# Kernel optimization log

Measured on AMD Instinct MI355X. Metric: run time of the kernel, lower is better.

Reference implementation:

```python
import jax, jax.numpy as jnp
import numpy as np

B, S, D, H, FFN = 2, 2048, 1024, 8, 4096
DK = D // H            # head key/query dim = 128
VD = 2 * D             # double_v_dim -> v_dim = 2048
DV = VD // H           # per-head value dim = 256
SCALE_BASE = 512.0
EPS = 1e-5


def _dup_interleave(m):
    # (S, d/2) -> (S, d), each column repeated twice adjacently
    return jnp.repeat(m, 2, axis=-1)


def _rotate_every_two(x):
    x1 = x[..., 0::2]
    x2 = x[..., 1::2]
    return jnp.stack((-x2, x1), axis=-1).reshape(x.shape)


def _xpos(x, downscale):
    # x: (B,H,S,d) -- XPOS rotary with length-dependent scale
    d = x.shape[-1]
    pos = jnp.arange(x.shape[-2], dtype=jnp.float32)
    sv = (jnp.arange(0, d, 2, dtype=jnp.float32) + 0.4 * d) / (1.4 * d)  # (d/2,)
    scale = sv[None, :] ** (pos / SCALE_BASE)[:, None]                    # (S, d/2)
    half = d // 2
    inv_freq = 1.0 / (10000.0 ** (jnp.arange(half, dtype=jnp.float32) / half))
    sinusoid = pos[:, None] * inv_freq[None, :]                           # (S, d/2)
    if downscale:
        scale = 1.0 / scale
    sin = _dup_interleave(jnp.sin(sinusoid) * scale)                      # (S, d)
    cos = _dup_interleave(jnp.cos(sinusoid) * scale)
    return x * cos + _rotate_every_two(x) * sin


def _gammas(heads):
    return 1.0 - jnp.exp(jnp.linspace(np.log(1 / 32), np.log(1 / 512), heads)).astype(jnp.float32)


def _layernorm(x, w, b):
    mu = jnp.mean(x, axis=-1, keepdims=True)
    var = jnp.var(x, axis=-1, keepdims=True)
    return (x - mu) * jax.lax.rsqrt(var + EPS) * w + b


def setup_inputs() -> dict:
    key = jax.random.key(0)
    ks = jax.random.split(key, 16)
    sD = 1.0 / np.sqrt(D)
    sF = 1.0 / np.sqrt(FFN)
    return {
        "X": jax.random.normal(ks[0], (B, S, D), jnp.float32),
        "Wq": jax.random.normal(ks[1], (H, D, DK), jnp.float32) * sD,
        "Wk": jax.random.normal(ks[2], (H, D, DK), jnp.float32) * sD,
        "Wv": jax.random.normal(ks[3], (H, D, DV), jnp.float32) * sD,
        "W_G": jax.random.normal(ks[4], (D, VD), jnp.float32) * sD,
        "W_O": jax.random.normal(ks[5], (VD, D), jnp.float32) / np.sqrt(VD),
        "gn_w": jnp.ones((VD,), jnp.float32),
        "gn_b": jnp.zeros((VD,), jnp.float32),
        "ln1_w": jnp.ones((D,), jnp.float32),
        "ln1_b": jnp.zeros((D,), jnp.float32),
        "ln2_w": jnp.ones((D,), jnp.float32),
        "ln2_b": jnp.zeros((D,), jnp.float32),
        "ffn_w1": jax.random.normal(ks[6], (D, FFN), jnp.float32) * sD,
        "ffn_b1": jnp.zeros((FFN,), jnp.float32),
        "ffn_w2": jax.random.normal(ks[7], (FFN, D), jnp.float32) * sF,
        "ffn_b2": jnp.zeros((D,), jnp.float32),
    }


def _retention(Xn, Wq, Wk, Wv, W_G, W_O, gn_w, gn_b):
    # Xn: (B,S,D) pre-normalized input
    Q = jnp.einsum("bsd,hdk->bhsk", Xn, Wq)
    K = jnp.einsum("bsd,hdk->bhsk", Xn, Wk)
    V = jnp.einsum("bsd,hdv->bhsv", Xn, Wv)
    Q = _xpos(Q, downscale=False)
    K = _xpos(K, downscale=True)
    # decay matrix D[h,n,m] = gamma_h^(n-m) for n>=m else 0
    n = jnp.arange(S)[:, None]
    m = jnp.arange(S)[None, :]
    mask = (n >= m)
    exponent = jnp.where(mask, (n - m).astype(jnp.float32), 0.0)
    g = _gammas(H)
    Dmat = jnp.where(mask[None], g[:, None, None] ** exponent[None], 0.0)  # (H,S,S)
    ret = jnp.einsum("bhsk,bhtk->bhst", Q, K) * Dmat[None]
    Y = jnp.einsum("bhst,bhtv->bhsv", ret, V)                              # (B,H,S,DV)
    Y = jnp.transpose(Y, (0, 2, 1, 3))                                     # (B,S,H,DV)
    # GroupNorm(heads, v_dim) applied per token: normalize within each head chunk
    mu = jnp.mean(Y, axis=-1, keepdims=True)
    var = jnp.var(Y, axis=-1, keepdims=True)
    Y = (Y - mu) * jax.lax.rsqrt(var + EPS)
    Y = Y.reshape(B, S, VD) * gn_w + gn_b
    G = Xn @ W_G
    gated = (G * jax.nn.sigmoid(G)) * Y                                     # swish gate
    return gated @ W_O


def reference(X, Wq, Wk, Wv, W_G, W_O, gn_w, gn_b, ln1_w, ln1_b, ln2_w, ln2_b,
              ffn_w1, ffn_b1, ffn_w2, ffn_b2):
    X = _retention(_layernorm(X, ln1_w, ln1_b), Wq, Wk, Wv, W_G, W_O, gn_w, gn_b) + X
    h = _layernorm(X, ln2_w, ln2_b)
    h = jax.nn.gelu(h @ ffn_w1 + ffn_b1, approximate=False) @ ffn_w2 + ffn_b2
    return h + X
```

## Files before the change

kernel.cpp:

```cpp
#include <hip/hip_runtime.h>
#include <hip/hip_bf16.h>

typedef unsigned short u16;
typedef unsigned int   u32;
typedef short short8 __attribute__((ext_vector_type(8)));
typedef float f32x4  __attribute__((ext_vector_type(4)));

__device__ __forceinline__ float b2f(u16 u) { return __uint_as_float(((u32)u) << 16); }
__device__ __forceinline__ u16 f2b(float f) {
    u32 u = __float_as_uint(f);
    u += 0x7FFF + ((u >> 16) & 1);
    return (u16)(u >> 16);
}

typedef const unsigned int __attribute__((address_space(1)))* gas1;
typedef unsigned int __attribute__((address_space(3)))* las3;
__device__ __forceinline__ void async_ld16(const void* g, const void* l) {
    __builtin_amdgcn_global_load_lds((gas1)(unsigned long long)g,
                                     (las3)(unsigned int)(unsigned long long)l,
                                     16, 0, 0);
}

__device__ __forceinline__ void wtrans_body(const float* __restrict__ W, u16* __restrict__ Wt,
                                            int K, int N, int bx, int by, int bz) {
    __shared__ u16 tile[32][36];
    const int k0 = bx * 32, n0 = by * 32;
    const float* Wz = W + (long)bz * K * N;
    u16* Wtz = Wt + (long)bz * K * N;
    const int t = threadIdx.x;
    const int r = t >> 3, c = (t & 7) * 4;
    float4 v = *(const float4*)(Wz + (long)(k0 + r) * N + n0 + c);
    tile[r][c+0] = f2b(v.x); tile[r][c+1] = f2b(v.y);
    tile[r][c+2] = f2b(v.z); tile[r][c+3] = f2b(v.w);
    __syncthreads();
    uint2 pk;
    pk.x = (u32)tile[c+0][r] | ((u32)tile[c+1][r] << 16);
    pk.y = (u32)tile[c+2][r] | ((u32)tile[c+3][r] << 16);
    *(uint2*)(Wtz + (long)(n0 + r) * K + k0 + c) = pk;
}

__device__ __forceinline__ void xtab_body(float4* __restrict__ tab, int blk) {
    int idx = blk * 256 + threadIdx.x;
    int j = idx & 63, s = idx >> 6;
    float sv = (2.f * j + 51.2f) / 179.2f;
    float scale = exp2f(log2f(sv) * ((float)s * (1.f / 512.f)));
    float inv_freq = exp2f((float)j * (-13.287712379549449f / 64.f));
    float ang = (float)s * inv_freq;
    float sn = sinf(ang), cs = cosf(ang);
    tab[idx] = make_float4(cs * scale, sn * scale, cs / scale, sn / scale);
}

__device__ __forceinline__ void ln_body(const float* __restrict__ X,
                                        const float* __restrict__ w,
                                        const float* __restrict__ bb,
                                        u16* __restrict__ out, long row) {
    const int t = threadIdx.x;
    float4 p = ((const float4*)(X + row * 1024))[t];
    float x[4] = { p.x, p.y, p.z, p.w };
    float s = x[0]+x[1]+x[2]+x[3];
    float q = x[0]*x[0]+x[1]*x[1]+x[2]*x[2]+x[3]*x[3];
#pragma unroll
    for (int o = 32; o > 0; o >>= 1) { s += __shfl_down(s, o, 64); q += __shfl_down(q, o, 64); }
    __shared__ float aS[4], aQ[4];
    if ((t & 63) == 0) { aS[t >> 6] = s; aQ[t >> 6] = q; }
    __syncthreads();
    s = aS[0]+aS[1]+aS[2]+aS[3];
    q = aQ[0]+aQ[1]+aQ[2]+aQ[3];
    float mean = s * (1.f/1024.f);
    float var  = q * (1.f/1024.f) - mean*mean;
    float rstd = rsqrtf(var + 1e-5f);
    float4 wv = ((const float4*)w)[t];
    float4 bv = ((const float4*)bb)[t];
    uint2 r;
    r.x = (u32)f2b((x[0]-mean)*rstd*wv.x + bv.x) | ((u32)f2b((x[1]-mean)*rstd*wv.y + bv.y) << 16);
    r.y = (u32)f2b((x[2]-mean)*rstd*wv.z + bv.z) | ((u32)f2b((x[3]-mean)*rstd*wv.w + bv.w) << 16);
    ((uint2*)(out + row * 1024))[t] = r;
}

__global__ __launch_bounds__(256) void prep_k(
    const float* __restrict__ Wq, const float* __restrict__ Wk,
    const float* __restrict__ Wv, const float* __restrict__ WG,
    const float* __restrict__ WO, const float* __restrict__ fw1,
    const float* __restrict__ fw2, const float* __restrict__ X,
    const float* __restrict__ ln1w, const float* __restrict__ ln1b,
    u16* __restrict__ WT, u16* __restrict__ WOT,
    u16* __restrict__ fw1T, u16* __restrict__ fw2T,
    float4* __restrict__ xtab, u16* __restrict__ Xn) {
    const int id = blockIdx.x;
    if (id < 16384) {
        const float* W; u16* Wt; int K, N, bx, by, bz = 0;
        if (id < 1024)       { W=Wq;  Wt=WT;           K=1024; N=128;  int l=id;       bx=l&31;  by=(l>>5)&3; bz=l>>7; }
        else if (id < 2048)  { W=Wk;  Wt=WT+1048576;   K=1024; N=128;  int l=id-1024;  bx=l&31;  by=(l>>5)&3; bz=l>>7; }
        else if (id < 4096)  { W=Wv;  Wt=WT+2097152;   K=1024; N=256;  int l=id-2048;  bx=l&31;  by=(l>>5)&7; bz=l>>8; }
        else if (id < 6144)  { W=WG;  Wt=WT+4194304;   K=1024; N=2048; int l=id-4096;  bx=l&31;  by=l>>5; }
        else if (id < 8192)  { W=WO;  Wt=WOT;          K=2048; N=1024; int l=id-6144;  bx=l&63;  by=l>>6; }
        else if (id < 12288) { W=fw1; Wt=fw1T;         K=1024; N=4096; int l=id-8192;  bx=l&31;  by=l>>5; }
        else                 { W=fw2; Wt=fw2T;         K=4096; N=1024; int l=id-12288; bx=l&127; by=l>>7; }
        wtrans_body(W, Wt, K, N, bx, by, bz);
    } else if (id < 16896) {
        xtab_body(xtab, id - 16384);
    } else {
        ln_body(X, ln1w, ln1b, Xn, id - 16896);
    }
}

__global__ __launch_bounds__(256) void ln2_combine(const float* __restrict__ P,
                                                   const float* __restrict__ X,
                                                   const float* __restrict__ w,
                                                   const float* __restrict__ bb,
                                                   float* __restrict__ X2,
                                                   u16* __restrict__ hb) {
    const long row = blockIdx.x;
    const int t = threadIdx.x;
    const float* p = P + row * 3072;
    float4 a = ((const float4*)p)[t];
    float4 c = ((const float4*)(p + 1024))[t];
    float4 xr = ((const float4*)(X + row * 1024))[t];
    float x[4] = { a.x+c.x+xr.x, a.y+c.y+xr.y, a.z+c.z+xr.z, a.w+c.w+xr.w };
    ((float4*)(X2 + row * 1024))[t] = make_float4(x[0], x[1], x[2], x[3]);
    float s = x[0]+x[1]+x[2]+x[3];
    float q = x[0]*x[0]+x[1]*x[1]+x[2]*x[2]+x[3]*x[3];
#pragma unroll
    for (int o = 32; o > 0; o >>= 1) { s += __shfl_down(s, o, 64); q += __shfl_down(q, o, 64); }
    __shared__ float aS[4], aQ[4];
    if ((t & 63) == 0) { aS[t >> 6] = s; aQ[t >> 6] = q; }
    __syncthreads();
    s = aS[0]+aS[1]+aS[2]+aS[3];
    q = aQ[0]+aQ[1]+aQ[2]+aQ[3];
    float mean = s * (1.f/1024.f);
    float var  = q * (1.f/1024.f) - mean*mean;
    float rstd = rsqrtf(var + 1e-5f);
    float4 wv = ((const float4*)w)[t];
    float4 bv = ((const float4*)bb)[t];
    uint2 r;
    r.x = (u32)f2b((x[0]-mean)*rstd*wv.x + bv.x) | ((u32)f2b((x[1]-mean)*rstd*wv.y + bv.y) << 16);
    r.y = (u32)f2b((x[2]-mean)*rstd*wv.z + bv.z) | ((u32)f2b((x[3]-mean)*rstd*wv.w + bv.w) << 16);
    ((uint2*)(hb + row * 1024))[t] = r;
}

__global__ __launch_bounds__(256) void ffn2_combine(const float* __restrict__ P,
                                                    const float* __restrict__ b2,
                                                    const float* __restrict__ X2,
                                                    float* __restrict__ out) {
    const long row = blockIdx.x;
    const int t = threadIdx.x;
    float4 p0 = ((const float4*)(P + row * 1024))[t];
    float4 p1 = ((const float4*)(P + 16777216 + row * 1024))[t];
    float4 x2 = ((const float4*)(X2 + row * 1024))[t];
    float4 bv = ((const float4*)b2)[t];
    ((float4*)(out + row * 1024))[t] = make_float4(
        p0.x + p1.x + x2.x + bv.x, p0.y + p1.y + x2.y + bv.y,
        p0.z + p1.z + x2.z + bv.z, p0.w + p1.w + x2.w + bv.w);
}

__global__ __launch_bounds__(256) void vtrans(const u16* __restrict__ Vseg, u16* __restrict__ Vt) {
    __shared__ u16 tile[32][36];
    const int s0 = blockIdx.x * 32, v0 = blockIdx.y * 32, z = blockIdx.z;
    const int b = z >> 3, h = z & 7;
    const u16* Vz = Vseg + (long)b * 2048 * 6144 + h * 256;
    u16* Vtz = Vt + (long)z * 256 * 2048;
    const int t = threadIdx.x;
    const int r = t >> 3, c = (t & 7) * 4;
    uint2 ld = *(const uint2*)(Vz + (long)(s0 + r) * 6144 + v0 + c);
    tile[r][c+0] = (u16)(ld.x & 0xFFFF); tile[r][c+1] = (u16)(ld.x >> 16);
    tile[r][c+2] = (u16)(ld.y & 0xFFFF); tile[r][c+3] = (u16)(ld.y >> 16);
    __syncthreads();
    uint2 pk;
    pk.x = (u32)tile[c+0][r] | ((u32)tile[c+1][r] << 16);
    pk.y = (u32)tile[c+2][r] | ((u32)tile[c+3][r] << 16);
    *(uint2*)(Vtz + (long)(v0 + r) * 2048 + s0 + c) = pk;
}

enum { EPI_GELU_BIAS = 2, EPI_QKVG = 4 };

template<int EPI>
__global__ __launch_bounds__(256) void mgemm(
    const u16* __restrict__ A, const u16* __restrict__ Bt, u16* __restrict__ Cv,
    int K, int aStride, long cStride,
    const float* __restrict__ bias) {
    __shared__ __align__(16) u16 As[2 * 128 * 32];
    __shared__ __align__(16) u16 Bs[2 * 128 * 32];
    const int pid = blockIdx.x;
    const int mb = pid & 31;
    const int nb = pid >> 5;
    const int t = threadIdx.x;
    const int row0 = mb * 128, col0 = nb * 128;
    const int wave = t >> 6, lane = t & 63;
    const int wm = wave >> 1, wn = wave & 1;
    const int quad = lane >> 4, l16 = lane & 15;
    const u16* Ag = A + (long)(row0 + (t >> 2)) * aStride + ((t & 3) * 8);
    const u16* Bg = Bt + (long)(col0 + (t >> 2)) * K + ((t & 3) * 8);
    const long aj = (long)64 * aStride;
    const long bj = (long)64 * K;
    const u32 lo = __builtin_amdgcn_readfirstlane((u32)(wave * 1024));

    f32x4 acc[4][4];
#pragma unroll
    for (int i = 0; i < 4; i++)
#pragma unroll
        for (int j = 0; j < 4; j++) acc[i][j] = (f32x4){0.f, 0.f, 0.f, 0.f};

    for (int k0 = 0; k0 < K; k0 += 64) {
#pragma unroll
        for (int h = 0; h < 2; h++) {
            const u16* Agh = Ag + k0 + h * 32;
            const u16* Bgh = Bg + k0 + h * 32;
            async_ld16(Agh,      (const char*)As + h*8192 + lo);
            async_ld16(Agh + aj, (const char*)As + h*8192 + 4096 + lo);
            async_ld16(Bgh,      (const char*)Bs + h*8192 + lo);
            async_ld16(Bgh + bj, (const char*)Bs + h*8192 + 4096 + lo);
        }
        __syncthreads();
#pragma unroll
        for (int h = 0; h < 2; h++) {
            short8 af[4], bf[4];
#pragma unroll
            for (int mt = 0; mt < 4; mt++)
                af[mt] = *(const short8*)(As + h*4096 + (wm*64 + mt*16 + l16) * 32 + quad*8);
#pragma unroll
            for (int nt = 0; nt < 4; nt++)
                bf[nt] = *(const short8*)(Bs + h*4096 + (wn*64 + nt*16 + l16) * 32 + quad*8);
#pragma unroll
            for (int mt = 0; mt < 4; mt++)
#pragma unroll
                for (int nt = 0; nt < 4; nt++)
                    acc[mt][nt] = __builtin_amdgcn_mfma_f32_16x16x32_bf16(af[mt], bf[nt], acc[mt][nt], 0, 0, 0);
        }
        __syncthreads();
    }

#pragma unroll
    for (int mt = 0; mt < 4; mt++) {
#pragma unroll
        for (int reg = 0; reg < 4; reg++) {
            int r = row0 + wm*64 + mt*16 + quad*4 + reg;
#pragma unroll
            for (int nt = 0; nt < 4; nt++) {
                int c = col0 + wn*64 + nt*16 + l16;
                float v = acc[mt][nt][reg];
                if constexpr (EPI == EPI_GELU_BIAS) {
                    v += bias[c];
                    v = 0.5f * v * (1.f + erff(v * 0.70710678118654752f));
                }
                float pv = __shfl_xor(v, 1, 64);
                float w0 = v, w1 = pv;
                if constexpr (EPI == EPI_QKVG) {
                    if (c < 2048) {
                        int j = (c & 127) >> 1;
                        float4 tb = ((const float4*)bias)[((r & 2047) << 6) + j];
                        float cs = (c < 1024) ? tb.x : tb.z;
                        float sn = (c < 1024) ? tb.y : tb.w;
                        w0 = v * cs - pv * sn;
                        w1 = pv * cs + v * sn;
                    }
                }
                if (!(lane & 1)) {
                    u32 pk = (u32)f2b(w0) | ((u32)f2b(w1) << 16);
                    *(u32*)(Cv + (long)r * cStride + c) = pk;
                }
            }
        }
    }
}

__global__ __launch_bounds__(256) void mgemm_sk(
    const u16* __restrict__ A, const u16* __restrict__ Bt, float* __restrict__ P,
    int K, int kHalf, int aStride, long pRowStride, long sliceOff) {
    __shared__ __align__(16) u16 As[2 * 128 * 32];
    __shared__ __align__(16) u16 Bs[2 * 128 * 32];
    const int pid = blockIdx.x;
    const int mb = pid & 31;
    const int nb = (pid & 255) >> 5;
    const int slice = pid >> 8;
    const int t = threadIdx.x;
    const int row0 = mb * 128, col0 = nb * 128;
    const int wave = t >> 6, lane = t & 63;
    const int wm = wave >> 1, wn = wave & 1;
    const int quad = lane >> 4, l16 = lane & 15;
    const u16* Ag = A + (long)(row0 + (t >> 2)) * aStride + ((t & 3) * 8);
    const u16* Bg = Bt + (long)(col0 + (t >> 2)) * K + ((t & 3) * 8);
    const long aj = (long)64 * aStride;
    const long bj = (long)64 * K;
    const u32 lo = __builtin_amdgcn_readfirstlane((u32)(wave * 1024));

    f32x4 acc[4][4];
#pragma unroll
    for (int i = 0; i < 4; i++)
#pragma unroll
        for (int j = 0; j < 4; j++) acc[i][j] = (f32x4){0.f, 0.f, 0.f, 0.f};

    const int kBeg = slice * kHalf, kEnd = kBeg + kHalf;
    for (int k0 = kBeg; k0 < kEnd; k0 += 64) {
#pragma unroll
        for (int h = 0; h < 2; h++) {
            const u16* Agh = Ag + k0 + h * 32;
            const u16* Bgh = Bg + k0 + h * 32;
            async_ld16(Agh,      (const char*)As + h*8192 + lo);
            async_ld16(Agh + aj, (const char*)As + h*8192 + 4096 + lo);
            async_ld16(Bgh,      (const char*)Bs + h*8192 + lo);
            async_ld16(Bgh + bj, (const char*)Bs + h*8192 + 4096 + lo);
        }
        __syncthreads();
#pragma unroll
        for (int h = 0; h < 2; h++) {
            short8 af[4], bf[4];
#pragma unroll
            for (int mt = 0; mt < 4; mt++)
                af[mt] = *(const short8*)(As + h*4096 + (wm*64 + mt*16 + l16) * 32 + quad*8);
#pragma unroll
            for (int nt = 0; nt < 4; nt++)
                bf[nt] = *(const short8*)(Bs + h*4096 + (wn*64 + nt*16 + l16) * 32 + quad*8);
#pragma unroll
            for (int mt = 0; mt < 4; mt++)
#pragma unroll
                for (int nt = 0; nt < 4; nt++)
                    acc[mt][nt] = __builtin_amdgcn_mfma_f32_16x16x32_bf16(af[mt], bf[nt], acc[mt][nt], 0, 0, 0);
        }
        __syncthreads();
    }

    float* Pb = P + slice * sliceOff;
#pragma unroll
    for (int mt = 0; mt < 4; mt++) {
#pragma unroll
        for (int reg = 0; reg < 4; reg++) {
            int r = row0 + wm*64 + mt*16 + quad*4 + reg;
#pragma unroll
            for (int nt = 0; nt < 4; nt++) {
                int c = col0 + wn*64 + nt*16 + l16;
                float v = acc[mt][nt][reg];
                float pv = __shfl_xor(v, 1, 64);
                if (!(lane & 1))
                    *(float2*)(Pb + (long)r * pRowStride + c) = make_float2(v, pv);
            }
        }
    }
}

__global__ __launch_bounds__(256) void retention_mfma(
    u16* __restrict__ QKVG, const u16* __restrict__ Vt,
    const float* __restrict__ gnw, const float* __restrict__ gnb) {
    __shared__ __align__(16) u16 Qs[4][64][32];
    __shared__ __align__(16) u16 Ks[2][4][32][32];
    __shared__ __align__(16) u16 Vs[2][256][32];
    __shared__ u16 Ss[64][40];
    const int id = blockIdx.x;
    const int halfg = id >> 8, r5 = id & 255;
    const int bh = r5 >> 4, i16 = r5 & 15;
    const int tile = halfg ? i16 : 31 - i16;
    const int b = bh >> 3, h = bh & 7;
    const int t = threadIdx.x;
    const int wave = t >> 6, lane = t & 63, quad = lane >> 4, l16 = lane & 15;
    const u32 lo = __builtin_amdgcn_readfirstlane((u32)(wave * 1024));
    const u16* Qbase = QKVG + (long)b * 2048 * 6144 + h * 128;
    const u16* Kbase = Qbase + 1024;
    const u16* Vbase = Vt + (long)(b * 8 + h) * 256 * 2048;
    u16* Gseg = QKVG + (long)b * 2048 * 6144 + 4096 + h * 256;

    float g = 1.f - expf(-3.4657359027997265f + (-0.3960841031771116f) * (float)h);
    float log2g = log2f(g);

    auto issueKV = [&](int jt, int buf) {
#pragma unroll
        for (int i = 0; i < 2; i++) {
            int c = t + i * 256;
            int ks = c >> 7, row = (c >> 2) & 31, cb = c & 3;
            async_ld16(Kbase + (long)(jt*32 + row) * 6144 + ks*32 + cb*8,
                       (const char*)Ks + buf*8192 + i*4096 + lo);
        }
#pragma unroll
        for (int i = 0; i < 4; i++) {
            int c = t + i * 256;
            int row = c >> 2, cb = c & 3;
            async_ld16(Vbase + (long)row * 2048 + jt*32 + cb*8,
                       (const char*)Vs + buf*16384 + i*4096 + lo);
        }
    };

#pragma unroll
    for (int i = 0; i < 4; i++) {
        int c = t + i * 256;
        int ks = c >> 8, row = (c >> 2) & 63, cb = c & 3;
        async_ld16(Qbase + (long)(tile*64 + row) * 6144 + ks*32 + cb*8,
                   (const char*)Qs + i*4096 + lo);
    }
    issueKV(0, 0);

    float gw[16], gbv[16];
#pragma unroll
    for (int nt = 0; nt < 16; nt++) {
        gw[nt]  = gnw[h*256 + nt*16 + l16];
        gbv[nt] = gnb[h*256 + nt*16 + l16];
    }
    f32x4 oacc[16];
#pragma unroll
    for (int nt = 0; nt < 16; nt++) oacc[nt] = (f32x4){0.f, 0.f, 0.f, 0.f};
    __syncthreads();

    const int njt = 2 * tile + 2;
    for (int jt = 0; jt < njt; jt++) {
        const int cur = jt & 1;
        if (jt + 1 < njt) issueKV(jt + 1, cur ^ 1);
        f32x4 s0 = (f32x4){0.f,0.f,0.f,0.f}, s1 = (f32x4){0.f,0.f,0.f,0.f};
#pragma unroll
        for (int ks = 0; ks < 4; ks++) {
            short8 aq = *(const short8*)&Qs[ks][wave*16 + l16][quad*8];
            short8 b0 = *(const short8*)&Ks[cur][ks][l16][quad*8];
            short8 b1 = *(const short8*)&Ks[cur][ks][16 + l16][quad*8];
            s0 = __builtin_amdgcn_mfma_f32_16x16x32_bf16(aq, b0, s0, 0, 0, 0);
            s1 = __builtin_amdgcn_mfma_f32_16x16x32_bf16(aq, b1, s1, 0, 0, 0);
        }
#pragma unroll
        for (int reg = 0; reg < 4; reg++) {
            int srow = tile*64 + wave*16 + quad*4 + reg;
            int tc0 = jt*32 + l16, tc1 = tc0 + 16;
            float d0 = (srow >= tc0) ? exp2f(log2g * (float)(srow - tc0)) : 0.f;
            float d1 = (srow >= tc1) ? exp2f(log2g * (float)(srow - tc1)) : 0.f;
            Ss[wave*16 + quad*4 + reg][l16]      = f2b(s0[reg] * d0);
            Ss[wave*16 + quad*4 + reg][16 + l16] = f2b(s1[reg] * d1);
        }
        short8 as = *(const short8*)&Ss[wave*16 + l16][quad*8];
#pragma unroll
        for (int nt = 0; nt < 16; nt++) {
            short8 bv = *(const short8*)&Vs[cur][nt*16 + l16][quad*8];
            oacc[nt] = __builtin_amdgcn_mfma_f32_16x16x32_bf16(as, bv, oacc[nt], 0, 0, 0);
        }
        __syncthreads();
    }

#pragma unroll
    for (int reg = 0; reg < 4; reg++) {
        float s = 0.f, q = 0.f;
#pragma unroll
        for (int nt = 0; nt < 16; nt++) { float v = oacc[nt][reg]; s += v; q += v*v; }
#pragma unroll
        for (int m = 1; m < 16; m <<= 1) { s += __shfl_xor(s, m, 16); q += __shfl_xor(q, m, 16); }
        float mean = s * (1.f/256.f);
        float var  = q * (1.f/256.f) - mean*mean;
        float rstd = rsqrtf(var + 1e-5f);
        int srow = tile*64 + wave*16 + quad*4 + reg;
        u16* grow = Gseg + (long)srow * 6144;
#pragma unroll
        for (int nt = 0; nt < 16; nt++) {
            float gval = b2f(grow[nt*16 + l16]);
            float y = (oacc[nt][reg] - mean) * rstd * gw[nt] + gbv[nt];
            float sg = gval / (1.f + expf(-gval));
            grow[nt*16 + l16] = f2b(sg * y);
        }
    }
}

extern "C" void kernel_launch(void* const* d_in, const int* in_sizes, int n_in,
                              void* d_out, int out_size, void* d_ws, size_t ws_size,
                              hipStream_t stream) {
    (void)in_sizes; (void)n_in; (void)out_size; (void)ws_size;
    const float* X    = (const float*)d_in[0];
    const float* Wq   = (const float*)d_in[1];
    const float* Wk   = (const float*)d_in[2];
    const float* Wv   = (const float*)d_in[3];
    const float* WG   = (const float*)d_in[4];
    const float* WO   = (const float*)d_in[5];
    const float* gnw  = (const float*)d_in[6];
    const float* gnb  = (const float*)d_in[7];
    const float* ln1w = (const float*)d_in[8];
    const float* ln1b = (const float*)d_in[9];
    const float* ln2w = (const float*)d_in[10];
    const float* ln2b = (const float*)d_in[11];
    const float* fw1  = (const float*)d_in[12];
    const float* fb1  = (const float*)d_in[13];
    const float* fw2  = (const float*)d_in[14];
    const float* fb2  = (const float*)d_in[15];

    constexpr int D = 1024, FFN = 4096;
    constexpr int M = 4096;
    constexpr long MB = 1048576;

    char* ws = (char*)d_ws;
    u16* WT   = (u16*)(ws + 0*MB);
    u16* WOT  = (u16*)(ws + 12*MB);
    u16* fw1T = (u16*)(ws + 16*MB);
    u16* fw2T = (u16*)(ws + 24*MB);
    u16*   QKVG = (u16*)(ws + 32*MB);
    u16*   Xn   = (u16*)(ws + 80*MB);
    float4* xtab= (float4*)(ws + 88*MB);
    u16*   Vt   = (u16*)(ws + 80*MB);
    float* X2   = (float*)(ws + 80*MB);
    u16*   hb   = (u16*)(ws + 0*MB);
    u16*   mid  = (u16*)(ws + 32*MB);
    float* PF   = (float*)(ws + 0*MB);

    prep_k<<<20992, 256, 0, stream>>>(Wq, Wk, Wv, WG, WO, fw1, fw2, X, ln1w, ln1b,
                                      WT, WOT, fw1T, fw2T, xtab, Xn);
    mgemm<EPI_QKVG><<<1536, 256, 0, stream>>>(
        Xn, WT, QKVG, D, D, 6144, (const float*)xtab);
    vtrans<<<dim3(64, 8, 16), 256, 0, stream>>>(QKVG + 2048, Vt);
    retention_mfma<<<512, 256, 0, stream>>>(QKVG, Vt, gnw, gnb);
    mgemm_sk<<<512, 256, 0, stream>>>(
        QKVG + 4096, WOT, (float*)QKVG, 2048, 1024, 6144, 3072, 1024);
    ln2_combine<<<M, 256, 0, stream>>>((const float*)QKVG, X, ln2w, ln2b, X2, hb);
    mgemm<EPI_GELU_BIAS><<<1024, 256, 0, stream>>>(
        hb, fw1T, mid, D, D, FFN, fb1);
    mgemm_sk<<<512, 256, 0, stream>>>(
        mid, fw2T, PF, 4096, 2048, 4096, 1024, 16777216);
    ffn2_combine<<<M, 256, 0, stream>>>(PF, fb2, X2, (float*)d_out);
}
```

Measured before the change: 493.0 us.

## Template GEMM K-panel depth, simplify epilogue stores, incrementally compute decay factors

Makes the number of K panels per barrier a template parameter, so the QKVG projection uses one 32-wide panel (half the shared memory, aiming for higher occupancy) while the FFN1 GEMM keeps two. Replaces the shuffle-and-pack paired stores in the GEMM epilogues with scalar per-lane stores, doing the rotary pairing through a single conditional shuffle. In the retention kernel, the per-element exp2 used for the decay mask is replaced by a running factor multiplied by precomputed gamma powers each tile. Risks include narrower, less coalesced global stores and accumulated float error in the running decay product.

```diff
diff --git a/kernel.cpp b/kernel.cpp
--- a/kernel.cpp
+++ b/kernel.cpp
@@ -173,13 +173,13 @@
 
 enum { EPI_GELU_BIAS = 2, EPI_QKVG = 4 };
 
-template<int EPI>
+template<int EPI, int PANELS>
 __global__ __launch_bounds__(256) void mgemm(
     const u16* __restrict__ A, const u16* __restrict__ Bt, u16* __restrict__ Cv,
     int K, int aStride, long cStride,
     const float* __restrict__ bias) {
-    __shared__ __align__(16) u16 As[2 * 128 * 32];
-    __shared__ __align__(16) u16 Bs[2 * 128 * 32];
+    __shared__ __align__(16) u16 As[PANELS * 4096];
+    __shared__ __align__(16) u16 Bs[PANELS * 4096];
     const int pid = blockIdx.x;
     const int mb = pid & 31;
     const int nb = pid >> 5;
@@ -200,9 +200,9 @@
 #pragma unroll
         for (int j = 0; j < 4; j++) acc[i][j] = (f32x4){0.f, 0.f, 0.f, 0.f};
 
-    for (int k0 = 0; k0 < K; k0 += 64) {
-#pragma unroll
-        for (int h = 0; h < 2; h++) {
+    for (int k0 = 0; k0 < K; k0 += PANELS * 32) {
+#pragma unroll
+        for (int h = 0; h < PANELS; h++) {
             const u16* Agh = Ag + k0 + h * 32;
             const u16* Bgh = Bg + k0 + h * 32;
             async_ld16(Agh,      (const char*)As + h*8192 + lo);
@@ -212,7 +212,7 @@
         }
         __syncthreads();
 #pragma unroll
-        for (int h = 0; h < 2; h++) {
+        for (int h = 0; h < PANELS; h++) {
             short8 af[4], bf[4];
 #pragma unroll
             for (int mt = 0; mt < 4; mt++)
@@ -241,23 +241,17 @@
                 if constexpr (EPI == EPI_GELU_BIAS) {
                     v += bias[c];
                     v = 0.5f * v * (1.f + erff(v * 0.70710678118654752f));
-                }
-                float pv = __shfl_xor(v, 1, 64);
-                float w0 = v, w1 = pv;
-                if constexpr (EPI == EPI_QKVG) {
+                } else if constexpr (EPI == EPI_QKVG) {
                     if (c < 2048) {
                         int j = (c & 127) >> 1;
                         float4 tb = ((const float4*)bias)[((r & 2047) << 6) + j];
                         float cs = (c < 1024) ? tb.x : tb.z;
                         float sn = (c < 1024) ? tb.y : tb.w;
-                        w0 = v * cs - pv * sn;
-                        w1 = pv * cs + v * sn;
+                        float partner = __shfl_xor(v, 1, 64);
+                        v = v * cs + ((c & 1) ? partner : -partner) * sn;
                     }
                 }
-                if (!(lane & 1)) {
-                    u32 pk = (u32)f2b(w0) | ((u32)f2b(w1) << 16);
-                    *(u32*)(Cv + (long)r * cStride + c) = pk;
-                }
+                Cv[(long)r * cStride + c] = f2b(v);
             }
         }
     }
@@ -266,8 +260,8 @@
 __global__ __launch_bounds__(256) void mgemm_sk(
     const u16* __restrict__ A, const u16* __restrict__ Bt, float* __restrict__ P,
     int K, int kHalf, int aStride, long pRowStride, long sliceOff) {
-    __shared__ __align__(16) u16 As[2 * 128 * 32];
-    __shared__ __align__(16) u16 Bs[2 * 128 * 32];
+    __shared__ __align__(16) u16 As[2 * 4096];
+    __shared__ __align__(16) u16 Bs[2 * 4096];
     const int pid = blockIdx.x;
     const int mb = pid & 31;
     const int nb = (pid & 255) >> 5;
@@ -328,10 +322,7 @@
 #pragma unroll
             for (int nt = 0; nt < 4; nt++) {
                 int c = col0 + wn*64 + nt*16 + l16;
-                float v = acc[mt][nt][reg];
-                float pv = __shfl_xor(v, 1, 64);
-                if (!(lane & 1))
-                    *(float2*)(Pb + (long)r * pRowStride + c) = make_float2(v, pv);
+                Pb[(long)r * pRowStride + c] = acc[mt][nt][reg];
             }
         }
     }
@@ -359,6 +350,11 @@
 
     float g = 1.f - expf(-3.4657359027997265f + (-0.3960841031771116f) * (float)h);
     float log2g = log2f(g);
+    const float gi16 = exp2f(log2g * -16.f);
+    const float gi32 = gi16 * gi16;
+    const float gf[4] = {1.f, g, g*g, g*g*g};
+    const int srow0 = tile*64 + wave*16 + quad*4;
+    float drun = exp2f(log2g * (float)(srow0 - l16));
 
     auto issueKV = [&](int jt, int buf) {
 #pragma unroll
@@ -412,13 +408,15 @@
         }
 #pragma unroll
         for (int reg = 0; reg < 4; reg++) {
-            int srow = tile*64 + wave*16 + quad*4 + reg;
+            int srow = srow0 + reg;
             int tc0 = jt*32 + l16, tc1 = tc0 + 16;
-            float d0 = (srow >= tc0) ? exp2f(log2g * (float)(srow - tc0)) : 0.f;
-            float d1 = (srow >= tc1) ? exp2f(log2g * (float)(srow - tc1)) : 0.f;
+            float dbase = drun * gf[reg];
+            float d0 = (srow >= tc0) ? dbase : 0.f;
+            float d1 = (srow >= tc1) ? dbase * gi16 : 0.f;
             Ss[wave*16 + quad*4 + reg][l16]      = f2b(s0[reg] * d0);
             Ss[wave*16 + quad*4 + reg][16 + l16] = f2b(s1[reg] * d1);
         }
+        drun *= gi32;
         short8 as = *(const short8*)&Ss[wave*16 + l16][quad*8];
 #pragma unroll
         for (int nt = 0; nt < 16; nt++) {
@@ -438,7 +436,7 @@
         float mean = s * (1.f/256.f);
         float var  = q * (1.f/256.f) - mean*mean;
         float rstd = rsqrtf(var + 1e-5f);
-        int srow = tile*64 + wave*16 + quad*4 + reg;
+        int srow = srow0 + reg;
         u16* grow = Gseg + (long)srow * 6144;
 #pragma unroll
         for (int nt = 0; nt < 16; nt++) {
@@ -491,14 +489,14 @@
 
     prep_k<<<20992, 256, 0, stream>>>(Wq, Wk, Wv, WG, WO, fw1, fw2, X, ln1w, ln1b,
                                       WT, WOT, fw1T, fw2T, xtab, Xn);
-    mgemm<EPI_QKVG><<<1536, 256, 0, stream>>>(
+    mgemm<EPI_QKVG, 1><<<1536, 256, 0, stream>>>(
         Xn, WT, QKVG, D, D, 6144, (const float*)xtab);
     vtrans<<<dim3(64, 8, 16), 256, 0, stream>>>(QKVG + 2048, Vt);
     retention_mfma<<<512, 256, 0, stream>>>(QKVG, Vt, gnw, gnb);
     mgemm_sk<<<512, 256, 0, stream>>>(
         QKVG + 4096, WOT, (float*)QKVG, 2048, 1024, 6144, 3072, 1024);
     ln2_combine<<<M, 256, 0, stream>>>((const float*)QKVG, X, ln2w, ln2b, X2, hb);
-    mgemm<EPI_GELU_BIAS><<<1024, 256, 0, stream>>>(
+    mgemm<EPI_GELU_BIAS, 2><<<1024, 256, 0, stream>>>(
         hb, fw1T, mid, D, D, FFN, fb1);
     mgemm_sk<<<512, 256, 0, stream>>>(
         mid, fw2T, PF, 4096, 2048, 4096, 1024, 16777216);
```

After: 472.3 us. 1.04x faster.
